# Optimization experiments

Hardware: AMD Instinct MI355X
Metric: run time of the kernel (lower is better)

The kernel has to match this reference:

```python
import jax, jax.numpy as jnp
import numpy as np

B, S, D, H, L = 2, 4096, 768, 12, 2
DH = D // H
W = 256            # one-sided sliding window (longformer-base attention_window=512)
VOCAB = 50265
SEP_ID = 2
N_SEPS = 63
G = N_SEPS + 1     # global tokens: <s> at pos 0 + all </s> separators
FF = 4 * D
C = 7
NEG = -1e9


def layer_norm(x, s, b, eps=1e-5):
    m = x.mean(-1, keepdims=True)
    v = ((x - m) ** 2).mean(-1, keepdims=True)
    return (x - m) * jax.lax.rsqrt(v + eps) * s + b


def setup_inputs():
    key = jax.random.key(0)
    keys = iter(jax.random.split(key, 64))
    def nrm(shape, sd=0.02):
        return jax.random.normal(next(keys), shape, jnp.float32) * sd
    input_ids = jax.random.randint(next(keys), (B, S), 5, VOCAB, dtype=jnp.int32)
    input_ids = input_ids.at[:, 0].set(0)  # <s>
    sep_pos = (jnp.arange(N_SEPS) + 1) * (S // (N_SEPS + 1))  # 64,128,...,4032
    input_ids = input_ids.at[:, sep_pos].set(SEP_ID)
    return dict(
        emb_tok=nrm((VOCAB, D)), emb_pos=nrm((S, D)),
        ln_e_s=jnp.ones((D,)), ln_e_b=jnp.zeros((D,)),
        Wq=nrm((L, D, D)), bq=jnp.zeros((L, D)),
        Wk=nrm((L, D, D)), bk=jnp.zeros((L, D)),
        Wv=nrm((L, D, D)), bv=jnp.zeros((L, D)),
        Wqg=nrm((L, D, D)), bqg=jnp.zeros((L, D)),
        Wkg=nrm((L, D, D)), bkg=jnp.zeros((L, D)),
        Wvg=nrm((L, D, D)), bvg=jnp.zeros((L, D)),
        Wo=nrm((L, D, D)), bo=jnp.zeros((L, D)),
        ln1_s=jnp.ones((L, D)), ln1_b=jnp.zeros((L, D)),
        Wf1=nrm((L, D, FF)), bf1=jnp.zeros((L, FF)),
        Wf2=nrm((L, FF, D)), bf2=jnp.zeros((L, D)),
        ln2_s=jnp.ones((L, D)), ln2_b=jnp.zeros((L, D)),
        Wc=nrm((D, C)), bc=jnp.zeros((C,)),
        input_ids=input_ids,
        attention_mask=jnp.ones((B, S), jnp.int32),
        left_overlap=2, right_overlap=2,
    )


def _forward(emb_tok, emb_pos, ln_e_s, ln_e_b, Wq, bq, Wk, bk, Wv, bv,
             Wqg, bqg, Wkg, bkg, Wvg, bvg, Wo, bo, ln1_s, ln1_b,
             Wf1, bf1, Wf2, bf2, ln2_s, ln2_b, Wc, bc,
             input_ids, attention_mask, left_overlap, right_overlap):
    pos = jnp.arange(S)
    # global attention mask: first token + every </s> token (as in the torch forward)
    g_mask = (input_ids == SEP_ID) | (pos[None, :] == 0)                         # [B,S]
    idx_g = jax.vmap(lambda m: jnp.nonzero(m, size=G, fill_value=0)[0])(g_mask)  # [B,G]
    am = attention_mask.astype(jnp.float32)
    key_local_ok = am * (1.0 - g_mask.astype(jnp.float32))  # globals excluded from windowed keys
    nb = S // W
    band_idx = jnp.arange(nb)[:, None] * W + jnp.arange(3 * W)[None, :]  # [nb,3W] into W-padded seq
    rel = jnp.arange(3 * W)[None, :] - W - jnp.arange(W)[:, None]        # key_pos - query_pos
    band_ok = (jnp.abs(rel) <= W)[None, None, None]                       # [1,1,1,W,3W]
    kv_ok = jnp.pad(key_local_ok, ((0, 0), (W, W)))[:, band_idx] > 0      # [B,nb,3W]
    mask = band_ok & kv_ok[:, None, :, None, :]                           # [B,1,nb,W,3W]
    scale = float(DH) ** -0.5
    bix = jnp.arange(B)[:, None]

    x = emb_tok[input_ids] + emb_pos[None]
    x = layer_norm(x, ln_e_s, ln_e_b)
    for l in range(L):
        q = (x @ Wq[l] + bq[l]).reshape(B, S, H, DH)
        k = (x @ Wk[l] + bk[l]).reshape(B, S, H, DH)
        v = (x @ Wv[l] + bv[l]).reshape(B, S, H, DH)
        kb = jnp.pad(k, ((0, 0), (W, W), (0, 0), (0, 0)))[:, band_idx]    # [B,nb,3W,H,DH]
        vb = jnp.pad(v, ((0, 0), (W, W), (0, 0), (0, 0)))[:, band_idx]
        s_band = jnp.einsum('bnqhd,bnkhd->bhnqk', q.reshape(B, nb, W, H, DH), kb) * scale
        s_band = jnp.where(mask, s_band, NEG)
        kg = jnp.take_along_axis(k, idx_g[:, :, None, None], axis=1)      # [B,G,H,DH]
        vg = jnp.take_along_axis(v, idx_g[:, :, None, None], axis=1)
        s_glob = jnp.einsum('bqhd,bghd->bhqg', q, kg) * scale
        probs = jax.nn.softmax(
            jnp.concatenate([s_band.reshape(B, H, S, 3 * W), s_glob], axis=-1), axis=-1)
        out = (jnp.einsum('bhnqk,bnkhd->bnqhd',
                          probs[..., :3 * W].reshape(B, H, nb, W, 3 * W), vb).reshape(B, S, H, DH)
               + jnp.einsum('bhqg,bghd->bqhd', probs[..., 3 * W:], vg)).reshape(B, S, D)
        # global query rows: full attention over all tokens with dedicated global projections
        xg = jnp.take_along_axis(x, idx_g[:, :, None], axis=1)            # [B,G,D]
        qg = (xg @ Wqg[l] + bqg[l]).reshape(B, G, H, DH)
        kga = (x @ Wkg[l] + bkg[l]).reshape(B, S, H, DH)
        vga = (x @ Wvg[l] + bvg[l]).reshape(B, S, H, DH)
        sg = jnp.where(am[:, None, None, :] > 0,
                       jnp.einsum('bghd,bshd->bhgs', qg, kga) * scale, NEG)
        og = jnp.einsum('bhgs,bshd->bghd', jax.nn.softmax(sg, axis=-1), vga).reshape(B, G, D)
        out = out.at[bix, idx_g].set(og)
        x = layer_norm(x + out @ Wo[l] + bo[l], ln1_s[l], ln1_b[l])
        x = layer_norm(x + jax.nn.gelu(x @ Wf1[l] + bf1[l]) @ Wf2[l] + bf2[l], ln2_s[l], ln2_b[l])
    # classification head (eval-mode dropout = identity). Faithful to the torch code,
    # which gathers hidden states at token POSITION j for j in [left, n_seps - right).
    core = x[:, left_overlap:N_SEPS - right_overlap, :]                    # [B, n_core, D]
    return (core @ Wc + bc).reshape(-1, C)


def reference(emb_tok, emb_pos, ln_e_s, ln_e_b, Wq, bq, Wk, bk, Wv, bv,
              Wqg, bqg, Wkg, bkg, Wvg, bvg, Wo, bo, ln1_s, ln1_b,
              Wf1, bf1, Wf2, bf2, ln2_s, ln2_b, Wc, bc,
              input_ids, attention_mask, left_overlap, right_overlap):
    return _forward(emb_tok, emb_pos, ln_e_s, ln_e_b, Wq, bq, Wk, bk, Wv, bv,
                    Wqg, bqg, Wkg, bkg, Wvg, bvg, Wo, bo, ln1_s, ln1_b,
                    Wf1, bf1, Wf2, bf2, ln2_s, ln2_b, Wc, bc,
                    input_ids, attention_mask, left_overlap, right_overlap)
```

## Files before the change

kernel.cpp:

```cpp
#include <hip/hip_runtime.h>
#include <hip/hip_bf16.h>
#include <stdint.h>

#define B_ 2
#define S_ 4096
#define D_ 768
#define H_ 12
#define DH_ 64
#define L_ 2
#define W_ 256
#define G_ 64
#define FF_ 3072
#define C_ 7
#define SEP_ 2
#define NEG_ (-1000000000.0f)
#define NC_ 16

typedef __attribute__((ext_vector_type(8))) short short8;
typedef __attribute__((ext_vector_type(4))) float f32x4;

__device__ __forceinline__ float bfu2f(unsigned short u) {
    return __uint_as_float(((unsigned int)u) << 16);
}
__device__ __forceinline__ unsigned short f2bfu(float f) {
    unsigned int x = __float_as_uint(f);
    unsigned int r = (x + 0x7fffu + ((x >> 16) & 1u)) >> 16;
    return (unsigned short)r;
}
__device__ __forceinline__ float gelu_tanh(float v) {
    float c = 0.7978845608028654f * (v + 0.044715f * v * v * v);
    return 0.5f * v * (1.0f + tanhf(c));
}

__device__ __forceinline__ void gl16(const unsigned short* g, unsigned short* l) {
    __builtin_amdgcn_global_load_lds(
        (const __attribute__((address_space(1))) unsigned int*)g,
        (__attribute__((address_space(3))) unsigned int*)l,
        16, 0, 0);
}

__device__ __forceinline__ void xcd_remap(int& bx, int& by, int& bz) {
    int nx = gridDim.x, ny = gridDim.y, nz = gridDim.z;
    int flat = bx + nx * (by + ny * bz);
    int nxz = nx * nz;
    int xcd = flat & 7;
    int n = flat >> 3;
    int band = n / nxz;
    int r = n - band * nxz;
    by = xcd * (ny >> 3) + band;
    bz = r / nx;
    bx = r - bz * nx;
}

#define GEMM_COMPUTE()                                                                   \
    {                                                                                    \
        short8 af[4], bf[4];                                                             \
        _Pragma("unroll")                                                                \
        for (int i_ = 0; i_ < 4; i_++)                                                   \
            af[i_] = *(const short8*)&As[(wm + i_ * 16 + l16) * 32 + quad * 8];          \
        _Pragma("unroll")                                                                \
        for (int j_ = 0; j_ < 4; j_++)                                                   \
            bf[j_] = *(const short8*)&Bs[(wn + j_ * 16 + l16) * 32 + quad * 8];          \
        _Pragma("unroll")                                                                \
        for (int i_ = 0; i_ < 4; i_++)                                                   \
            _Pragma("unroll")                                                            \
            for (int j_ = 0; j_ < 4; j_++)                                               \
                acc[i_][j_] = __builtin_amdgcn_mfma_f32_16x16x32_bf16(af[i_], bf[j_],    \
                                                                      acc[i_][j_], 0, 0, 0); \
    }

__global__ __launch_bounds__(256) void k_wtrans(
    const float* __restrict__ src, unsigned short* __restrict__ dst,
    int K, int N, size_t dstStride) {
    int l = blockIdx.z;
    src += (size_t)l * K * N;
    dst += (size_t)l * dstStride;
    __shared__ unsigned short tile[32][36];
    int t = threadIdx.x;
    int r = t >> 3, c4 = (t & 7) << 2;
    int k0 = blockIdx.y << 5, n0 = blockIdx.x << 5;
    float4 v = *(const float4*)(src + (size_t)(k0 + r) * N + n0 + c4);
    tile[c4 + 0][r] = f2bfu(v.x);
    tile[c4 + 1][r] = f2bfu(v.y);
    tile[c4 + 2][r] = f2bfu(v.z);
    tile[c4 + 3][r] = f2bfu(v.w);
    __syncthreads();
    ushort4 o;
    o.x = tile[r][c4 + 0]; o.y = tile[r][c4 + 1];
    o.z = tile[r][c4 + 2]; o.w = tile[r][c4 + 3];
    *(ushort4*)(dst + (size_t)(n0 + r) * K + k0 + c4) = o;
}

__global__ __launch_bounds__(256) void k_embed_ln(
    const int* __restrict__ ids, const float* __restrict__ etok,
    const float* __restrict__ epos, const float* __restrict__ lns,
    const float* __restrict__ lnb, float* __restrict__ x,
    unsigned short* __restrict__ xb) {
    int row = (blockIdx.x << 2) + (threadIdx.x >> 6);
    int lane = threadIdx.x & 63;
    int s = row & (S_ - 1);
    int id = ids[row];
    const float4* ep = (const float4*)(etok + (size_t)id * D_);
    const float4* pp = (const float4*)(epos + (size_t)s * D_);
    float4 a[3];
    float sum = 0.f, sum2 = 0.f;
#pragma unroll
    for (int i = 0; i < 3; i++) {
        float4 ev = ep[lane + i * 64];
        float4 pv = pp[lane + i * 64];
        ev.x += pv.x; ev.y += pv.y; ev.z += pv.z; ev.w += pv.w;
        a[i] = ev;
        sum  += ev.x + ev.y + ev.z + ev.w;
        sum2 += ev.x * ev.x + ev.y * ev.y + ev.z * ev.z + ev.w * ev.w;
    }
#pragma unroll
    for (int off = 1; off < 64; off <<= 1) {
        sum += __shfl_xor(sum, off);
        sum2 += __shfl_xor(sum2, off);
    }
    float mean = sum * (1.0f / D_);
    float var = sum2 * (1.0f / D_) - mean * mean;
    float rs = rsqrtf(var + 1e-5f);
    float4* xp = (float4*)(x + (size_t)row * D_);
#pragma unroll
    for (int i = 0; i < 3; i++) {
        float4 g = *(const float4*)(lns + lane * 4 + i * 256);
        float4 bb = *(const float4*)(lnb + lane * 4 + i * 256);
        float4 v;
        v.x = (a[i].x - mean) * rs * g.x + bb.x;
        v.y = (a[i].y - mean) * rs * g.y + bb.y;
        v.z = (a[i].z - mean) * rs * g.z + bb.z;
        v.w = (a[i].w - mean) * rs * g.w + bb.w;
        xp[lane + i * 64] = v;
        ushort4 u; u.x = f2bfu(v.x); u.y = f2bfu(v.y); u.z = f2bfu(v.z); u.w = f2bfu(v.w);
        *(ushort4*)(xb + (size_t)row * D_ + lane * 4 + i * 256) = u;
    }
}

__global__ __launch_bounds__(256) void k_add_ln(
    float* __restrict__ x, const float* __restrict__ y, const float* __restrict__ y2,
    const float* __restrict__ lns, const float* __restrict__ lnb,
    unsigned short* __restrict__ xb) {
    int row = (blockIdx.x << 2) + (threadIdx.x >> 6);
    int lane = threadIdx.x & 63;
    float4* xp = (float4*)(x + (size_t)row * D_);
    const float4* yp = (const float4*)(y + (size_t)row * D_);
    const float4* y2p = y2 ? (const float4*)(y2 + (size_t)row * D_) : nullptr;
    float4 a[3];
    float sum = 0.f, sum2 = 0.f;
#pragma unroll
    for (int i = 0; i < 3; i++) {
        float4 xv = xp[lane + i * 64];
        float4 yv = yp[lane + i * 64];
        xv.x += yv.x; xv.y += yv.y; xv.z += yv.z; xv.w += yv.w;
        if (y2p) {
            float4 zv = y2p[lane + i * 64];
            xv.x += zv.x; xv.y += zv.y; xv.z += zv.z; xv.w += zv.w;
        }
        a[i] = xv;
        sum  += xv.x + xv.y + xv.z + xv.w;
        sum2 += xv.x * xv.x + xv.y * xv.y + xv.z * xv.z + xv.w * xv.w;
    }
#pragma unroll
    for (int off = 1; off < 64; off <<= 1) {
        sum += __shfl_xor(sum, off);
        sum2 += __shfl_xor(sum2, off);
    }
    float mean = sum * (1.0f / D_);
    float var = sum2 * (1.0f / D_) - mean * mean;
    float rs = rsqrtf(var + 1e-5f);
#pragma unroll
    for (int i = 0; i < 3; i++) {
        float4 g = *(const float4*)(lns + lane * 4 + i * 256);
        float4 bb = *(const float4*)(lnb + lane * 4 + i * 256);
        float4 v;
        v.x = (a[i].x - mean) * rs * g.x + bb.x;
        v.y = (a[i].y - mean) * rs * g.y + bb.y;
        v.z = (a[i].z - mean) * rs * g.z + bb.z;
        v.w = (a[i].w - mean) * rs * g.w + bb.w;
        xp[lane + i * 64] = v;
        ushort4 u; u.x = f2bfu(v.x); u.y = f2bfu(v.y); u.z = f2bfu(v.z); u.w = f2bfu(v.w);
        *(ushort4*)(xb + (size_t)row * D_ + lane * 4 + i * 256) = u;
    }
}

__global__ __launch_bounds__(256) void k_idx(const int* __restrict__ ids, int* __restrict__ idxg) {
    int b = blockIdx.x;
    int t = threadIdx.x;
    __shared__ int cnt[256];
    __shared__ int totsh;
    int loc[16];
    int n = 0;
#pragma unroll
    for (int i = 0; i < 16; i++) {
        int s = t * 16 + i;
        if (s == 0 || ids[b * S_ + s] == SEP_) loc[n++] = s;
    }
    cnt[t] = n;
    __syncthreads();
    int base = 0;
    for (int u = 0; u < t; u++) base += cnt[u];
    for (int i = 0; i < n; i++) {
        int o = base + i;
        if (o < G_) idxg[b * G_ + o] = loc[i];
    }
    if (t == 255) totsh = base + n;
    __syncthreads();
    if (t == 0)
        for (int o = totsh; o < G_; o++) idxg[b * G_ + o] = 0;
}

__global__ __launch_bounds__(256) void k_gemm_mfma(
    const unsigned short* __restrict__ A, const unsigned short* __restrict__ Wt,
    const float* __restrict__ Wf, const float* __restrict__ bias,
    float* __restrict__ Cf, float* __restrict__ Cf2, unsigned short* __restrict__ Cb,
    int M, int N, int K, int act) {
    __shared__ __align__(16) unsigned short As[128 * 32];
    __shared__ __align__(16) unsigned short Bs[128 * 32];
    int bx = blockIdx.x, by = blockIdx.y, bz = blockIdx.z;
    xcd_remap(bx, by, bz);
    int t = threadIdx.x;
    int wave = t >> 6, lane = t & 63, l16 = lane & 15, quad = lane >> 4;
    int m0 = by << 7, n0 = bx << 7;
    int wm = (wave >> 1) << 6, wn = (wave & 1) << 6;
    int slice = bz;
    int kper = K / gridDim.z;
    int kbeg = slice * kper, kend = kbeg + kper;
    f32x4 acc[4][4];
#pragma unroll
    for (int i = 0; i < 4; i++)
#pragma unroll
        for (int j = 0; j < 4; j++) acc[i][j] = (f32x4){0.f, 0.f, 0.f, 0.f};

    int ch = wave * 128 + lane;
    int srow = ch >> 2, spos = ch & 3;
    unsigned short* al0 = As + wave * 1024;
    unsigned short* al1 = As + wave * 1024 + 512;
    unsigned short* bl0 = Bs + wave * 1024;
    unsigned short* bl1 = Bs + wave * 1024 + 512;
    const unsigned short* ag = A + (size_t)(m0 + srow) * K + kbeg + spos * 8;

    if (Wt) {
        const unsigned short* bg = Wt + (size_t)(n0 + srow) * K + kbeg + spos * 8;
        for (int k0 = kbeg; k0 < kend; k0 += 32) {
            gl16(ag, al0);
            gl16(ag + (size_t)16 * K, al1);
            gl16(bg, bl0);
            gl16(bg + (size_t)16 * K, bl1);
            __syncthreads();
            GEMM_COMPUTE();
            __syncthreads();
            ag += 32; bg += 32;
        }
    } else {
        int bn = t & 127, bkh = (t >> 7) << 4;
        for (int k0 = kbeg; k0 < kend; k0 += 32) {
            gl16(ag, al0);
            gl16(ag + (size_t)16 * K, al1);
            const float* bp = Wf + (size_t)(k0 + bkh) * N + n0 + bn;
            unsigned int pk[8];
#pragma unroll
            for (int i = 0; i < 8; i++) {
                unsigned int lo = f2bfu(bp[(size_t)(2 * i) * N]);
                unsigned int hi = f2bfu(bp[(size_t)(2 * i + 1) * N]);
                pk[i] = lo | (hi << 16);
            }
            *(uint4*)&Bs[bn * 32 + bkh] = *(uint4*)&pk[0];
            *(uint4*)&Bs[bn * 32 + bkh + 8] = *(uint4*)&pk[4];
            __syncthreads();
            GEMM_COMPUTE();
            __syncthreads();
            ag += 32;
        }
    }
    float bj[4];
#pragma unroll
    for (int j = 0; j < 4; j++) bj[j] = (slice == 0) ? bias[n0 + wn + j * 16 + l16] : 0.f;
    float* outp = (slice == 0) ? Cf : Cf2;
#pragma unroll
    for (int i = 0; i < 4; i++)
#pragma unroll
        for (int j = 0; j < 4; j++) {
            int col = n0 + wn + j * 16 + l16;
#pragma unroll
            for (int r = 0; r < 4; r++) {
                int row = m0 + wm + i * 16 + quad * 4 + r;
                float v = acc[i][j][r] + bj[j];
                if (act) v = gelu_tanh(v);
                if (outp) outp[(size_t)row * N + col] = v;
                else      Cb[(size_t)row * N + col] = f2bfu(v);
            }
        }
}

struct P5 {
    const unsigned short* Wt[5];
    const float* Wf[5];
    const float* bias[5];
    unsigned short* out[5];
};
__global__ __launch_bounds__(256) void k_gemm_qkv5(
    const unsigned short* __restrict__ A, P5 p) {
    __shared__ __align__(16) unsigned short As[128 * 32];
    __shared__ __align__(16) unsigned short Bs[128 * 32];
    int bx = blockIdx.x, by = blockIdx.y, bz = blockIdx.z;
    xcd_remap(bx, by, bz);
    const unsigned short* __restrict__ Wt = p.Wt[bz];
    const float* __restrict__ Wf = p.Wf[bz];
    const float* __restrict__ bias = p.bias[bz];
    unsigned short* __restrict__ Cb = p.out[bz];
    const int N = D_, K = D_;
    int t = threadIdx.x;
    int wave = t >> 6, lane = t & 63, l16 = lane & 15, quad = lane >> 4;
    int m0 = by << 7, n0 = bx << 7;
    int wm = (wave >> 1) << 6, wn = (wave & 1) << 6;
    f32x4 acc[4][4];
#pragma unroll
    for (int i = 0; i < 4; i++)
#pragma unroll
        for (int j = 0; j < 4; j++) acc[i][j] = (f32x4){0.f, 0.f, 0.f, 0.f};

    int ch = wave * 128 + lane;
    int srow = ch >> 2, spos = ch & 3;
    unsigned short* al0 = As + wave * 1024;
    unsigned short* al1 = As + wave * 1024 + 512;
    unsigned short* bl0 = Bs + wave * 1024;
    unsigned short* bl1 = Bs + wave * 1024 + 512;
    const unsigned short* ag = A + (size_t)(m0 + srow) * K + spos * 8;

    if (Wt) {
        const unsigned short* bg = Wt + (size_t)(n0 + srow) * K + spos * 8;
        for (int k0 = 0; k0 < K; k0 += 32) {
            gl16(ag + k0, al0);
            gl16(ag + 16 * K + k0, al1);
            gl16(bg + k0, bl0);
            gl16(bg + 16 * K + k0, bl1);
            __syncthreads();
            GEMM_COMPUTE();
            __syncthreads();
        }
    } else {
        int bn = t & 127, bkh = (t >> 7) << 4;
        for (int k0 = 0; k0 < K; k0 += 32) {
            gl16(ag + k0, al0);
            gl16(ag + 16 * K + k0, al1);
            const float* bp = Wf + (size_t)(k0 + bkh) * N + n0 + bn;
            unsigned int pk[8];
#pragma unroll
            for (int i = 0; i < 8; i++) {
                unsigned int lo = f2bfu(bp[(size_t)(2 * i) * N]);
                unsigned int hi = f2bfu(bp[(size_t)(2 * i + 1) * N]);
                pk[i] = lo | (hi << 16);
            }
            *(uint4*)&Bs[bn * 32 + bkh] = *(uint4*)&pk[0];
            *(uint4*)&Bs[bn * 32 + bkh + 8] = *(uint4*)&pk[4];
            __syncthreads();
            GEMM_COMPUTE();
            __syncthreads();
        }
    }
    float bj[4];
#pragma unroll
    for (int j = 0; j < 4; j++) bj[j] = bias[n0 + wn + j * 16 + l16];
#pragma unroll
    for (int i = 0; i < 4; i++)
#pragma unroll
        for (int j = 0; j < 4; j++) {
            int col = n0 + wn + j * 16 + l16;
#pragma unroll
            for (int r = 0; r < 4; r++) {
                int row = m0 + wm + i * 16 + quad * 4 + r;
                float v = acc[i][j][r] + bj[j];
                size_t adr = ((((size_t)(row >> 12)) * H_ + (col >> 6)) * S_ +
                              (row & (S_ - 1))) * DH_ + (col & 63);
                Cb[adr] = f2bfu(v);
            }
        }
}

__global__ __launch_bounds__(256) void k_lattn(
    const unsigned short* __restrict__ q, const unsigned short* __restrict__ k,
    const unsigned short* __restrict__ v, const int* __restrict__ ids,
    const int* __restrict__ am, const int* __restrict__ idxg,
    unsigned short* __restrict__ Tb) {
    int s0 = blockIdx.x << 6, h = blockIdx.y, b = blockIdx.z;
    int t = threadIdx.x;
    int wave = t >> 6, lane = t & 63, l16 = lane & 15, quad = lane >> 4;

    __shared__ unsigned short Ks[64][72];
    __shared__ unsigned short Vt[64][72];
    __shared__ unsigned short Ps[64][72];
    __shared__ unsigned char keyok[64];

    const size_t headbase = (((size_t)b * H_) + h) * S_;
    int qrow = s0 + wave * 16 + l16;
    const unsigned short* qptr = q + (headbase + qrow) * DH_;
    short8 qa0 = *(const short8*)(qptr + quad * 8);
    short8 qa1 = *(const short8*)(qptr + 32 + quad * 8);

    f32x4 O[4];
#pragma unroll
    for (int nf = 0; nf < 4; nf++) O[nf] = (f32x4){0.f, 0.f, 0.f, 0.f};
    float m_run[4] = {-3.4e38f, -3.4e38f, -3.4e38f, -3.4e38f};
    float l_run[4] = {0.f, 0.f, 0.f, 0.f};

    int kbase = s0 - 256;
    int sr = t >> 2, sc = t & 3;

    for (int tile = 0; tile < 10; tile++) {
        int sK, sclamp; bool okf;
        if (tile < 9) {
            sK = kbase + tile * 64 + sr;
            bool inr = (sK >= 0) && (sK < S_);
            sclamp = inr ? sK : 0;
            okf = inr && (am[b * S_ + sclamp] != 0) &&
                  !((ids[b * S_ + sclamp] == SEP_) || (sK == 0));
        } else {
            sK = idxg[b * G_ + sr];
            sclamp = sK; okf = true;
        }
        if (sc == 0) keyok[sr] = okf ? 1 : 0;
        const unsigned short* srcK = k + (headbase + sclamp) * DH_;
        const unsigned short* srcV = v + (headbase + sclamp) * DH_;
        uint4 k0v = *(const uint4*)(srcK + sc * 8);
        uint4 k1v = *(const uint4*)(srcK + (sc + 4) * 8);
        uint4 v0v = *(const uint4*)(srcV + sc * 8);
        uint4 v1v = *(const uint4*)(srcV + (sc + 4) * 8);
        *(uint4*)&Ks[sr][sc * 8] = k0v;
        *(uint4*)&Ks[sr][(sc + 4) * 8] = k1v;
        const unsigned int* vw0 = (const unsigned int*)&v0v;
        const unsigned int* vw1 = (const unsigned int*)&v1v;
#pragma unroll
        for (int i = 0; i < 4; i++) {
            Vt[sc * 8 + 2 * i][sr]      = (unsigned short)(vw0[i] & 0xffff);
            Vt[sc * 8 + 2 * i + 1][sr]  = (unsigned short)(vw0[i] >> 16);
            Vt[(sc + 4) * 8 + 2 * i][sr]     = (unsigned short)(vw1[i] & 0xffff);
            Vt[(sc + 4) * 8 + 2 * i + 1][sr] = (unsigned short)(vw1[i] >> 16);
        }
        __syncthreads();

        f32x4 Sf[4];
#pragma unroll
        for (int nf = 0; nf < 4; nf++) {
            short8 b0 = *(const short8*)&Ks[nf * 16 + l16][quad * 8];
            short8 b1 = *(const short8*)&Ks[nf * 16 + l16][32 + quad * 8];
            f32x4 a = (f32x4){0.f, 0.f, 0.f, 0.f};
            a = __builtin_amdgcn_mfma_f32_16x16x32_bf16(qa0, b0, a, 0, 0, 0);
            a = __builtin_amdgcn_mfma_f32_16x16x32_bf16(qa1, b1, a, 0, 0, 0);
            Sf[nf] = a;
        }
        int ktb = kbase + tile * 64;
        bool kval[4];
#pragma unroll
        for (int nf = 0; nf < 4; nf++) kval[nf] = (tile == 9) || (keyok[nf * 16 + l16] != 0);
        float P_[4][4];
        float mt[4];
#pragma unroll
        for (int r = 0; r < 4; r++) {
            int qs = s0 + wave * 16 + quad * 4 + r;
            float mx = -3.4e38f;
#pragma unroll
            for (int nf = 0; nf < 4; nf++) {
                int ks2 = ktb + nf * 16 + l16;
                bool ok = kval[nf] && ((tile == 9) || (ks2 >= qs - 256 && ks2 <= qs + 256));
                float sv = ok ? Sf[nf][r] * 0.125f : NEG_;
                P_[nf][r] = sv;
                mx = fmaxf(mx, sv);
            }
            mt[r] = mx;
        }
#pragma unroll
        for (int off = 1; off < 16; off <<= 1)
#pragma unroll
            for (int r = 0; r < 4; r++) mt[r] = fmaxf(mt[r], __shfl_xor(mt[r], off));
        float alpha[4], lt[4];
#pragma unroll
        for (int r = 0; r < 4; r++) {
            float mn = fmaxf(m_run[r], mt[r]);
            alpha[r] = __expf(m_run[r] - mn);
            m_run[r] = mn; lt[r] = 0.f;
        }
#pragma unroll
        for (int nf = 0; nf < 4; nf++)
#pragma unroll
            for (int r = 0; r < 4; r++) {
                float p = (P_[nf][r] > -1.0e8f) ? __expf(P_[nf][r] - m_run[r]) : 0.f;
                P_[nf][r] = p; lt[r] += p;
            }
#pragma unroll
        for (int off = 1; off < 16; off <<= 1)
#pragma unroll
            for (int r = 0; r < 4; r++) lt[r] += __shfl_xor(lt[r], off);
#pragma unroll
        for (int r = 0; r < 4; r++) l_run[r] = l_run[r] * alpha[r] + lt[r];
#pragma unroll
        for (int nf = 0; nf < 4; nf++) {
            O[nf][0] *= alpha[0]; O[nf][1] *= alpha[1];
            O[nf][2] *= alpha[2]; O[nf][3] *= alpha[3];
        }
#pragma unroll
        for (int nf = 0; nf < 4; nf++)
#pragma unroll
            for (int r = 0; r < 4; r++)
                Ps[wave * 16 + quad * 4 + r][nf * 16 + l16] = f2bfu(P_[nf][r]);
#pragma unroll
        for (int hh = 0; hh < 2; hh++) {
            short8 pa = *(const short8*)&Ps[wave * 16 + l16][hh * 32 + quad * 8];
#pragma unroll
            for (int nf = 0; nf < 4; nf++) {
                short8 vb8 = *(const short8*)&Vt[nf * 16 + l16][hh * 32 + quad * 8];
                O[nf] = __builtin_amdgcn_mfma_f32_16x16x32_bf16(pa, vb8, O[nf], 0, 0, 0);
            }
        }
        __syncthreads();
    }
#pragma unroll
    for (int r = 0; r < 4; r++) {
        int qs = s0 + wave * 16 + quad * 4 + r;
        float invl = 1.0f / l_run[r];
        size_t base = ((size_t)(b * S_ + qs)) * D_ + h * DH_;
#pragma unroll
        for (int nf = 0; nf < 4; nf++)
            Tb[base + nf * 16 + l16] = f2bfu(O[nf][r] * invl);
    }
}

__global__ __launch_bounds__(256) void k_gattn_part(
    const unsigned short* __restrict__ qg, const unsigned short* __restrict__ kga,
    const unsigned short* __restrict__ vga, const int* __restrict__ am,
    float* __restrict__ Opart, float* __restrict__ mbuf, float* __restrict__ lbuf) {
    int c = blockIdx.x, h = blockIdx.y, b = blockIdx.z;
    int t = threadIdx.x;
    int wave = t >> 6, lane = t & 63, l16 = lane & 15, quad = lane >> 4;

    __shared__ unsigned short Ks[64][72];
    __shared__ unsigned short Vt[64][72];
    __shared__ unsigned short Ps[64][72];
    __shared__ unsigned char keyok[64];

    const size_t headbase = (((size_t)b * H_) + h) * S_;
    int grow = wave * 16 + l16;
    const unsigned short* qptr = qg + ((size_t)(b * G_ + grow)) * D_ + h * DH_;
    short8 qa0 = *(const short8*)(qptr + quad * 8);
    short8 qa1 = *(const short8*)(qptr + 32 + quad * 8);

    f32x4 O[4];
#pragma unroll
    for (int nf = 0; nf < 4; nf++) O[nf] = (f32x4){0.f, 0.f, 0.f, 0.f};
    float m_run[4] = {-3.4e38f, -3.4e38f, -3.4e38f, -3.4e38f};
    float l_run[4] = {0.f, 0.f, 0.f, 0.f};

    int kbase = c * 256;
    int sr = t >> 2, sc = t & 3;

    for (int tile = 0; tile < 4; tile++) {
        int sK = kbase + tile * 64 + sr;
        if (sc == 0) keyok[sr] = (am[b * S_ + sK] != 0) ? 1 : 0;
        const unsigned short* srcK = kga + (headbase + sK) * DH_;
        const unsigned short* srcV = vga + (headbase + sK) * DH_;
        uint4 k0v = *(const uint4*)(srcK + sc * 8);
        uint4 k1v = *(const uint4*)(srcK + (sc + 4) * 8);
        uint4 v0v = *(const uint4*)(srcV + sc * 8);
        uint4 v1v = *(const uint4*)(srcV + (sc + 4) * 8);
        *(uint4*)&Ks[sr][sc * 8] = k0v;
        *(uint4*)&Ks[sr][(sc + 4) * 8] = k1v;
        const unsigned int* vw0 = (const unsigned int*)&v0v;
        const unsigned int* vw1 = (const unsigned int*)&v1v;
#pragma unroll
        for (int i = 0; i < 4; i++) {
            Vt[sc * 8 + 2 * i][sr]      = (unsigned short)(vw0[i] & 0xffff);
            Vt[sc * 8 + 2 * i + 1][sr]  = (unsigned short)(vw0[i] >> 16);
            Vt[(sc + 4) * 8 + 2 * i][sr]     = (unsigned short)(vw1[i] & 0xffff);
            Vt[(sc + 4) * 8 + 2 * i + 1][sr] = (unsigned short)(vw1[i] >> 16);
        }
        __syncthreads();

        f32x4 Sf[4];
#pragma unroll
        for (int nf = 0; nf < 4; nf++) {
            short8 b0 = *(const short8*)&Ks[nf * 16 + l16][quad * 8];
            short8 b1 = *(const short8*)&Ks[nf * 16 + l16][32 + quad * 8];
            f32x4 a = (f32x4){0.f, 0.f, 0.f, 0.f};
            a = __builtin_amdgcn_mfma_f32_16x16x32_bf16(qa0, b0, a, 0, 0, 0);
            a = __builtin_amdgcn_mfma_f32_16x16x32_bf16(qa1, b1, a, 0, 0, 0);
            Sf[nf] = a;
        }
        bool kval[4];
#pragma unroll
        for (int nf = 0; nf < 4; nf++) kval[nf] = (keyok[nf * 16 + l16] != 0);
        float P_[4][4];
        float mt[4];
#pragma unroll
        for (int r = 0; r < 4; r++) {
            float mx = -3.4e38f;
#pragma unroll
            for (int nf = 0; nf < 4; nf++) {
                float sv = kval[nf] ? Sf[nf][r] * 0.125f : NEG_;
                P_[nf][r] = sv;
                mx = fmaxf(mx, sv);
            }
            mt[r] = mx;
        }
#pragma unroll
        for (int off = 1; off < 16; off <<= 1)
#pragma unroll
            for (int r = 0; r < 4; r++) mt[r] = fmaxf(mt[r], __shfl_xor(mt[r], off));
        float alpha[4], lt[4];
#pragma unroll
        for (int r = 0; r < 4; r++) {
            float mn = fmaxf(m_run[r], mt[r]);
            alpha[r] = __expf(m_run[r] - mn);
            m_run[r] = mn; lt[r] = 0.f;
        }
#pragma unroll
        for (int nf = 0; nf < 4; nf++)
#pragma unroll
            for (int r = 0; r < 4; r++) {
                float p = (P_[nf][r] > -1.0e8f) ? __expf(P_[nf][r] - m_run[r]) : 0.f;
                P_[nf][r] = p; lt[r] += p;
            }
#pragma unroll
        for (int off = 1; off < 16; off <<= 1)
#pragma unroll
            for (int r = 0; r < 4; r++) lt[r] += __shfl_xor(lt[r], off);
#pragma unroll
        for (int r = 0; r < 4; r++) l_run[r] = l_run[r] * alpha[r] + lt[r];
#pragma unroll
        for (int nf = 0; nf < 4; nf++) {
            O[nf][0] *= alpha[0]; O[nf][1] *= alpha[1];
            O[nf][2] *= alpha[2]; O[nf][3] *= alpha[3];
        }
#pragma unroll
        for (int nf = 0; nf < 4; nf++)
#pragma unroll
            for (int r = 0; r < 4; r++)
                Ps[wave * 16 + quad * 4 + r][nf * 16 + l16] = f2bfu(P_[nf][r]);
#pragma unroll
        for (int hh = 0; hh < 2; hh++) {
            short8 pa = *(const short8*)&Ps[wave * 16 + l16][hh * 32 + quad * 8];
#pragma unroll
            for (int nf = 0; nf < 4; nf++) {
                short8 vb8 = *(const short8*)&Vt[nf * 16 + l16][hh * 32 + quad * 8];
                O[nf] = __builtin_amdgcn_mfma_f32_16x16x32_bf16(pa, vb8, O[nf], 0, 0, 0);
            }
        }
        __syncthreads();
    }
    size_t bhc = ((size_t)(b * H_ + h)) * NC_ + c;
#pragma unroll
    for (int r = 0; r < 4; r++) {
        int row = wave * 16 + quad * 4 + r;
#pragma unroll
        for (int nf = 0; nf < 4; nf++)
            Opart[bhc * (G_ * DH_) + (size_t)row * DH_ + nf * 16 + l16] = O[nf][r];
        if (l16 == 0) {
            mbuf[bhc * G_ + row] = m_run[r];
            lbuf[bhc * G_ + row] = l_run[r];
        }
    }
}

__global__ __launch_bounds__(64) void k_gattn_comb(
    const float* __restrict__ Opart, const float* __restrict__ mbuf,
    const float* __restrict__ lbuf, const int* __restrict__ idxg,
    unsigned short* __restrict__ Tb) {
    int g = blockIdx.x, h = blockIdx.y, b = blockIdx.z;
    int d = threadIdx.x;
    size_t bh = (size_t)(b * H_ + h);
    float M = -3.4e38f;
    float mv[NC_];
#pragma unroll
    for (int c = 0; c < NC_; c++) {
        mv[c] = mbuf[(bh * NC_ + c) * G_ + g];
        M = fmaxf(M, mv[c]);
    }
    float L = 0.f, o = 0.f;
#pragma unroll
    for (int c = 0; c < NC_; c++) {
        float e = __expf(mv[c] - M);
        L += lbuf[(bh * NC_ + c) * G_ + g] * e;
        o += Opart[(bh * NC_ + c) * (G_ * DH_) + (size_t)g * DH_ + d] * e;
    }
    int srow = idxg[b * G_ + g];
    Tb[((size_t)(b * S_ + srow)) * D_ + h * DH_ + d] = f2bfu(o / L);
}

__global__ __launch_bounds__(256) void k_gemm(
    const float* __restrict__ A, const float* __restrict__ Bw,
    const float* __restrict__ bias, float* __restrict__ Cf,
    unsigned short* __restrict__ Cb, int M, int N, int K, int act) {
    __shared__ float As[16][68];
    __shared__ float Bs[16][68];
    int tl = threadIdx.x;
    int tx = tl & 15, ty = tl >> 4;
    int m0 = blockIdx.y << 6, n0 = blockIdx.x << 6;
    float c[4][4] = {{0.f}};
    int arow = tl >> 2, akk = (tl & 3) << 2;
    int bkk = tl >> 4, bcol = (tl & 15) << 2;
    for (int k0 = 0; k0 < K; k0 += 16) {
        float4 a4 = *(const float4*)(A + (size_t)(m0 + arow) * K + k0 + akk);
        As[akk + 0][arow] = a4.x; As[akk + 1][arow] = a4.y;
        As[akk + 2][arow] = a4.z; As[akk + 3][arow] = a4.w;
        float4 b4 = *(const float4*)(Bw + (size_t)(k0 + bkk) * N + n0 + bcol);
        Bs[bkk][bcol + 0] = b4.x; Bs[bkk][bcol + 1] = b4.y;
        Bs[bkk][bcol + 2] = b4.z; Bs[bkk][bcol + 3] = b4.w;
        __syncthreads();
#pragma unroll
        for (int kk = 0; kk < 16; kk++) {
            float4 av = *(const float4*)&As[kk][ty << 2];
            float4 bv = *(const float4*)&Bs[kk][tx << 2];
            float aa[4] = {av.x, av.y, av.z, av.w};
            float bb[4] = {bv.x, bv.y, bv.z, bv.w};
#pragma unroll
            for (int i = 0; i < 4; i++)
#pragma unroll
                for (int j = 0; j < 4; j++) c[i][j] += aa[i] * bb[j];
        }
        __syncthreads();
    }
    float bias4[4];
#pragma unroll
    for (int j = 0; j < 4; j++) bias4[j] = bias[n0 + (tx << 2) + j];
#pragma unroll
    for (int i = 0; i < 4; i++) {
        int mrow = m0 + (ty << 2) + i;
        float v0 = c[i][0] + bias4[0], v1 = c[i][1] + bias4[1];
        float v2 = c[i][2] + bias4[2], v3 = c[i][3] + bias4[3];
        if (act) { v0 = gelu_tanh(v0); v1 = gelu_tanh(v1); v2 = gelu_tanh(v2); v3 = gelu_tanh(v3); }
        if (Cf) {
            float4 o; o.x = v0; o.y = v1; o.z = v2; o.w = v3;
            *(float4*)(Cf + (size_t)mrow * N + n0 + (tx << 2)) = o;
        } else {
            ushort4 o; o.x = f2bfu(v0); o.y = f2bfu(v1); o.z = f2bfu(v2); o.w = f2bfu(v3);
            *(ushort4*)(Cb + (size_t)mrow * N + n0 + (tx << 2)) = o;
        }
    }
}

__global__ __launch_bounds__(256) void k_gather_xg(
    const float* __restrict__ x, const int* __restrict__ idxg, float* __restrict__ xg) {
    int bg = blockIdx.x;
    int b = bg / G_;
    int srow = idxg[bg];
    for (int d = threadIdx.x; d < D_; d += 256)
        xg[(size_t)bg * D_ + d] = x[((size_t)(b * S_ + srow)) * D_ + d];
}

__global__ __launch_bounds__(256) void k_classifier(
    const float* __restrict__ x, const float* __restrict__ Wc,
    const float* __restrict__ bc, const int* __restrict__ lo_p,
    int rows_pb, float* __restrict__ out) {
    int r = blockIdx.x;
    int b = r / rows_pb, i = r % rows_pb;
    int s = lo_p[0] + i;
    int t = threadIdx.x;
    __shared__ float xr[D_];
    __shared__ float red[256];
    const float* xrow = x + ((size_t)(b * S_ + s)) * D_;
    for (int d = t; d < D_; d += 256) xr[d] = xrow[d];
    __syncthreads();
    for (int c = 0; c < C_; c++) {
        float loc = 0.f;
        for (int d = t; d < D_; d += 256) loc += xr[d] * Wc[d * C_ + c];
        red[t] = loc; __syncthreads();
        for (int o = 128; o; o >>= 1) { if (t < o) red[t] += red[t + o]; __syncthreads(); }
        if (t == 0) out[r * C_ + c] = red[0] + bc[c];
        __syncthreads();
    }
}

extern "C" void kernel_launch(void* const* d_in, const int* in_sizes, int n_in,
                              void* d_out, int out_size, void* d_ws, size_t ws_size,
                              hipStream_t stream) {
    (void)in_sizes; (void)n_in;
    const float* emb_tok = (const float*)d_in[0];
    const float* emb_pos = (const float*)d_in[1];
    const float* ln_e_s = (const float*)d_in[2];
    const float* ln_e_b = (const float*)d_in[3];
    const float* Wq  = (const float*)d_in[4];
    const float* bq  = (const float*)d_in[5];
    const float* Wk  = (const float*)d_in[6];
    const float* bk  = (const float*)d_in[7];
    const float* Wv  = (const float*)d_in[8];
    const float* bv  = (const float*)d_in[9];
    const float* Wqg = (const float*)d_in[10];
    const float* bqg = (const float*)d_in[11];
    const float* Wkg = (const float*)d_in[12];
    const float* bkg = (const float*)d_in[13];
    const float* Wvg = (const float*)d_in[14];
    const float* bvg = (const float*)d_in[15];
    const float* Wo  = (const float*)d_in[16];
    const float* bo  = (const float*)d_in[17];
    const float* ln1_s = (const float*)d_in[18];
    const float* ln1_b = (const float*)d_in[19];
    const float* Wf1 = (const float*)d_in[20];
    const float* bf1 = (const float*)d_in[21];
    const float* Wf2 = (const float*)d_in[22];
    const float* bf2 = (const float*)d_in[23];
    const float* ln2_s = (const float*)d_in[24];
    const float* ln2_b = (const float*)d_in[25];
    const float* Wc  = (const float*)d_in[26];
    const float* bc  = (const float*)d_in[27];
    const int* input_ids = (const int*)d_in[28];
    const int* attn_mask = (const int*)d_in[29];
    const int* lo        = (const int*)d_in[30];

    const size_t SZB = (size_t)B_ * S_ * D_;
    const size_t D2 = (size_t)D_ * D_;
    const size_t PL = 6 * D2 + 2 * (size_t)D_ * FF_;
    uint8_t* w = (uint8_t*)d_ws;
    float*          x    = (float*)w;
    unsigned short* xb   = (unsigned short*)(w + 4 * SZB);
    float*          P    = (float*)(w + 6 * SZB);
    unsigned short* qb   = (unsigned short*)(w + 10 * SZB);
    unsigned short* kb   = (unsigned short*)(w + 12 * SZB);
    unsigned short* vb   = (unsigned short*)(w + 14 * SZB);
    unsigned short* kgab = (unsigned short*)(w + 16 * SZB);
    unsigned short* vgab = (unsigned short*)(w + 18 * SZB);
    unsigned short* Hb   = (unsigned short*)(w + 10 * SZB);
    unsigned short* Tb   = (unsigned short*)(w + 20 * SZB);
    float* xg = (float*)(w + 22 * SZB);
    unsigned short* qgb = (unsigned short*)(w + 22 * SZB + (size_t)B_ * G_ * D_ * 4);
    int* idxg = (int*)(w + 22 * SZB + (size_t)B_ * G_ * D_ * 4 + (size_t)B_ * G_ * D_ * 2);
    float* Opart = (float*)(w + 23 * SZB);
    float* mbuf  = (float*)(w + 24 * SZB);
    float* lbuf  = mbuf + (size_t)B_ * H_ * NC_ * G_;

    const size_t P2_OFF = 24 * SZB + (1u << 20);
    const size_t WB_OFF = P2_OFF + 4 * SZB;
    const size_t NEED_P2 = WB_OFF;
    const size_t NEED_W = WB_OFF + L_ * PL * 2;
    float* P2 = (float*)(w + P2_OFF);
    unsigned short* wb = (unsigned short*)(w + WB_OFF);
    const int useW = (ws_size >= NEED_W) ? 1 : 0;
    const int useSplit = (ws_size >= NEED_P2) ? 1 : 0;

    const int BS = B_ * S_;

    if (useW) {
        k_wtrans<<<dim3(D_/32, D_/32, L_), 256, 0, stream>>>(Wq,  wb + 0*D2, D_, D_, PL);
        k_wtrans<<<dim3(D_/32, D_/32, L_), 256, 0, stream>>>(Wk,  wb + 1*D2, D_, D_, PL);
        k_wtrans<<<dim3(D_/32, D_/32, L_), 256, 0, stream>>>(Wv,  wb + 2*D2, D_, D_, PL);
        k_wtrans<<<dim3(D_/32, D_/32, L_), 256, 0, stream>>>(Wkg, wb + 3*D2, D_, D_, PL);
        k_wtrans<<<dim3(D_/32, D_/32, L_), 256, 0, stream>>>(Wvg, wb + 4*D2, D_, D_, PL);
        k_wtrans<<<dim3(D_/32, D_/32, L_), 256, 0, stream>>>(Wo,  wb + 5*D2, D_, D_, PL);
        k_wtrans<<<dim3(FF_/32, D_/32, L_), 256, 0, stream>>>(Wf1, wb + 6*D2, D_, FF_, PL);
        k_wtrans<<<dim3(D_/32, FF_/32, L_), 256, 0, stream>>>(Wf2, wb + 6*D2 + (size_t)D_*FF_, FF_, D_, PL);
    }

    k_embed_ln<<<BS / 4, 256, 0, stream>>>(input_ids, emb_tok, emb_pos, ln_e_s, ln_e_b, x, xb);
    k_idx<<<B_, 256, 0, stream>>>(input_ids, idxg);

    dim3 g_d(D_ / 128, BS / 128);
    dim3 g_ds(D_ / 128, BS / 128, useSplit ? 2 : 1);
    dim3 g_d5(D_ / 128, BS / 128, 5);
    dim3 g_ff(FF_ / 128, BS / 128);
    dim3 g_qg(D_ / 64, (B_ * G_) / 64);

    for (int l = 0; l < L_; l++) {
        const unsigned short* wbl = wb + (size_t)l * PL;
        P5 p5;
        p5.Wf[0] = Wq  + (size_t)l * D2;  p5.bias[0] = bq  + l * D_;  p5.out[0] = qb;
        p5.Wf[1] = Wk  + (size_t)l * D2;  p5.bias[1] = bk  + l * D_;  p5.out[1] = kb;
        p5.Wf[2] = Wv  + (size_t)l * D2;  p5.bias[2] = bv  + l * D_;  p5.out[2] = vb;
        p5.Wf[3] = Wkg + (size_t)l * D2;  p5.bias[3] = bkg + l * D_;  p5.out[3] = kgab;
        p5.Wf[4] = Wvg + (size_t)l * D2;  p5.bias[4] = bvg + l * D_;  p5.out[4] = vgab;
        for (int i = 0; i < 5; i++) p5.Wt[i] = useW ? (wbl + (size_t)i * D2) : nullptr;
        const float* Wqg_l = Wqg + (size_t)l * D2;
        const float* Wo_l  = Wo  + (size_t)l * D2;
        const float* Wf1_l = Wf1 + (size_t)l * D_ * FF_;
        const float* Wf2_l = Wf2 + (size_t)l * FF_ * D_;
        const unsigned short* Wo_t  = useW ? (wbl + 5 * D2) : nullptr;
        const unsigned short* Wf1_t = useW ? (wbl + 6 * D2) : nullptr;
        const unsigned short* Wf2_t = useW ? (wbl + 6 * D2 + (size_t)D_ * FF_) : nullptr;

        k_gemm_qkv5<<<g_d5, 256, 0, stream>>>(xb, p5);
        k_lattn<<<dim3(S_ / 64, H_, B_), 256, 0, stream>>>(qb, kb, vb, input_ids, attn_mask, idxg, Tb);
        k_gather_xg<<<B_ * G_, 256, 0, stream>>>(x, idxg, xg);
        k_gemm<<<g_qg, 256, 0, stream>>>(xg, Wqg_l, bqg + l * D_, nullptr, qgb, B_ * G_, D_, D_, 0);
        k_gattn_part<<<dim3(NC_, H_, B_), 256, 0, stream>>>(qgb, kgab, vgab, attn_mask, Opart, mbuf, lbuf);
        k_gattn_comb<<<dim3(G_, H_, B_), 64, 0, stream>>>(Opart, mbuf, lbuf, idxg, Tb);
        k_gemm_mfma<<<g_ds, 256, 0, stream>>>(Tb, Wo_t, Wo_l, bo + l * D_, P, P2, nullptr, BS, D_, D_, 0);
        k_add_ln<<<BS / 4, 256, 0, stream>>>(x, P, useSplit ? P2 : nullptr, ln1_s + l * D_, ln1_b + l * D_, xb);
        k_gemm_mfma<<<g_ff, 256, 0, stream>>>(xb, Wf1_t, Wf1_l, bf1 + l * FF_, nullptr, nullptr, Hb, BS, FF_, D_, 1);
        k_gemm_mfma<<<g_ds, 256, 0, stream>>>(Hb, Wf2_t, Wf2_l, bf2 + l * D_, P, P2, nullptr, BS, D_, FF_, 0);
        k_add_ln<<<BS / 4, 256, 0, stream>>>(x, P, useSplit ? P2 : nullptr, ln2_s + l * D_, ln2_b + l * D_, xb);
    }

    int rows = out_size / C_;
    int rows_pb = rows / B_;
    k_classifier<<<rows, 256, 0, stream>>>(x, Wc, bc, lo, rows_pb, (float*)d_out);
}
```

Before: 1.160 ms.

## Double-buffer LDS tiles in MFMA GEMMs and use exp-based GELU

The bf16 pre-transposed weight paths of the generic and QKV GEMM kernels now keep two LDS buffers. The next K-slice is issued via global_load_lds while MFMAs run on the current one, and there is one vmcnt wait plus barrier per iteration instead of two syncthreads. This aims to hide global-load latency behind compute, at the cost of doubling LDS use per block, which may lower occupancy. GELU-tanh is also rewritten as the equivalent sigmoid form v/(1+exp(-2c)) using the fast __expf intrinsic to cheapen the FFN epilogue, with slightly different rounding.

```diff
diff --git a/kernel.cpp b/kernel.cpp
--- a/kernel.cpp
+++ b/kernel.cpp
@@ -28,8 +28,8 @@
     return (unsigned short)r;
 }
 __device__ __forceinline__ float gelu_tanh(float v) {
-    float c = 0.7978845608028654f * (v + 0.044715f * v * v * v);
-    return 0.5f * v * (1.0f + tanhf(c));
+    float u = 1.5957691216057308f * v + 0.0713548162726f * v * v * v;
+    return v / (1.0f + __expf(-u));
 }
 
 __device__ __forceinline__ void gl16(const unsigned short* g, unsigned short* l) {
@@ -52,21 +52,27 @@
     bx = r - bz * nx;
 }
 
-#define GEMM_COMPUTE()                                                                   \
+#define GEMM_COMPUTE(Ab, Bb)                                                             \
     {                                                                                    \
         short8 af[4], bf[4];                                                             \
         _Pragma("unroll")                                                                \
         for (int i_ = 0; i_ < 4; i_++)                                                   \
-            af[i_] = *(const short8*)&As[(wm + i_ * 16 + l16) * 32 + quad * 8];          \
+            af[i_] = *(const short8*)&(Ab)[(wm + i_ * 16 + l16) * 32 + quad * 8];        \
         _Pragma("unroll")                                                                \
         for (int j_ = 0; j_ < 4; j_++)                                                   \
-            bf[j_] = *(const short8*)&Bs[(wn + j_ * 16 + l16) * 32 + quad * 8];          \
+            bf[j_] = *(const short8*)&(Bb)[(wn + j_ * 16 + l16) * 32 + quad * 8];        \
         _Pragma("unroll")                                                                \
         for (int i_ = 0; i_ < 4; i_++)                                                   \
             _Pragma("unroll")                                                            \
             for (int j_ = 0; j_ < 4; j_++)                                               \
                 acc[i_][j_] = __builtin_amdgcn_mfma_f32_16x16x32_bf16(af[i_], bf[j_],    \
                                                                       acc[i_][j_], 0, 0, 0); \
+    }
+
+#define WAIT_VM0_BARRIER()                                   \
+    {                                                        \
+        asm volatile("s_waitcnt vmcnt(0)" ::: "memory");     \
+        __builtin_amdgcn_s_barrier();                        \
     }
 
 __global__ __launch_bounds__(256) void k_wtrans(
@@ -215,8 +221,8 @@
     const float* __restrict__ Wf, const float* __restrict__ bias,
     float* __restrict__ Cf, float* __restrict__ Cf2, unsigned short* __restrict__ Cb,
     int M, int N, int K, int act) {
-    __shared__ __align__(16) unsigned short As[128 * 32];
-    __shared__ __align__(16) unsigned short Bs[128 * 32];
+    __shared__ __align__(16) unsigned short As[2 * 128 * 32];
+    __shared__ __align__(16) unsigned short Bs[2 * 128 * 32];
     int bx = blockIdx.x, by = blockIdx.y, bz = blockIdx.z;
     xcd_remap(bx, by, bz);
     int t = threadIdx.x;
@@ -234,29 +240,36 @@
 
     int ch = wave * 128 + lane;
     int srow = ch >> 2, spos = ch & 3;
-    unsigned short* al0 = As + wave * 1024;
-    unsigned short* al1 = As + wave * 1024 + 512;
-    unsigned short* bl0 = Bs + wave * 1024;
-    unsigned short* bl1 = Bs + wave * 1024 + 512;
     const unsigned short* ag = A + (size_t)(m0 + srow) * K + kbeg + spos * 8;
 
     if (Wt) {
         const unsigned short* bg = Wt + (size_t)(n0 + srow) * K + kbeg + spos * 8;
+        gl16(ag, As + wave * 1024);
+        gl16(ag + (size_t)16 * K, As + wave * 1024 + 512);
+        gl16(bg, Bs + wave * 1024);
+        gl16(bg + (size_t)16 * K, Bs + wave * 1024 + 512);
+        WAIT_VM0_BARRIER();
+        int cur = 0;
         for (int k0 = kbeg; k0 < kend; k0 += 32) {
-            gl16(ag, al0);
-            gl16(ag + (size_t)16 * K, al1);
-            gl16(bg, bl0);
-            gl16(bg + (size_t)16 * K, bl1);
-            __syncthreads();
-            GEMM_COMPUTE();
-            __syncthreads();
-            ag += 32; bg += 32;
+            int koff = k0 + 32 - kbeg;
+            if (k0 + 32 < kend) {
+                int nb = cur ^ 1;
+                gl16(ag + koff, As + nb * 4096 + wave * 1024);
+                gl16(ag + koff + (size_t)16 * K, As + nb * 4096 + wave * 1024 + 512);
+                gl16(bg + koff, Bs + nb * 4096 + wave * 1024);
+                gl16(bg + koff + (size_t)16 * K, Bs + nb * 4096 + wave * 1024 + 512);
+            }
+            const unsigned short* Ab = As + cur * 4096;
+            const unsigned short* Bb = Bs + cur * 4096;
+            GEMM_COMPUTE(Ab, Bb);
+            WAIT_VM0_BARRIER();
+            cur ^= 1;
         }
     } else {
         int bn = t & 127, bkh = (t >> 7) << 4;
         for (int k0 = kbeg; k0 < kend; k0 += 32) {
-            gl16(ag, al0);
-            gl16(ag + (size_t)16 * K, al1);
+            gl16(ag + (k0 - kbeg), As + wave * 1024);
+            gl16(ag + (k0 - kbeg) + (size_t)16 * K, As + wave * 1024 + 512);
             const float* bp = Wf + (size_t)(k0 + bkh) * N + n0 + bn;
             unsigned int pk[8];
 #pragma unroll
@@ -268,9 +281,8 @@
             *(uint4*)&Bs[bn * 32 + bkh] = *(uint4*)&pk[0];
             *(uint4*)&Bs[bn * 32 + bkh + 8] = *(uint4*)&pk[4];
             __syncthreads();
-            GEMM_COMPUTE();
+            GEMM_COMPUTE(As, Bs);
             __syncthreads();
-            ag += 32;
         }
     }
     float bj[4];
@@ -301,8 +313,8 @@
 };
 __global__ __launch_bounds__(256) void k_gemm_qkv5(
     const unsigned short* __restrict__ A, P5 p) {
-    __shared__ __align__(16) unsigned short As[128 * 32];
-    __shared__ __align__(16) unsigned short Bs[128 * 32];
+    __shared__ __align__(16) unsigned short As[2 * 128 * 32];
+    __shared__ __align__(16) unsigned short Bs[2 * 128 * 32];
     int bx = blockIdx.x, by = blockIdx.y, bz = blockIdx.z;
     xcd_remap(bx, by, bz);
     const unsigned short* __restrict__ Wt = p.Wt[bz];
@@ -322,28 +334,36 @@
 
     int ch = wave * 128 + lane;
     int srow = ch >> 2, spos = ch & 3;
-    unsigned short* al0 = As + wave * 1024;
-    unsigned short* al1 = As + wave * 1024 + 512;
-    unsigned short* bl0 = Bs + wave * 1024;
-    unsigned short* bl1 = Bs + wave * 1024 + 512;
     const unsigned short* ag = A + (size_t)(m0 + srow) * K + spos * 8;
 
     if (Wt) {
         const unsigned short* bg = Wt + (size_t)(n0 + srow) * K + spos * 8;
+        gl16(ag, As + wave * 1024);
+        gl16(ag + (size_t)16 * K, As + wave * 1024 + 512);
+        gl16(bg, Bs + wave * 1024);
+        gl16(bg + (size_t)16 * K, Bs + wave * 1024 + 512);
+        WAIT_VM0_BARRIER();
+        int cur = 0;
         for (int k0 = 0; k0 < K; k0 += 32) {
-            gl16(ag + k0, al0);
-            gl16(ag + 16 * K + k0, al1);
-            gl16(bg + k0, bl0);
-            gl16(bg + 16 * K + k0, bl1);
-            __syncthreads();
-            GEMM_COMPUTE();
-            __syncthreads();
+            int koff = k0 + 32;
+            if (koff < K) {
+                int nb = cur ^ 1;
+                gl16(ag + koff, As + nb * 4096 + wave * 1024);
+                gl16(ag + koff + (size_t)16 * K, As + nb * 4096 + wave * 1024 + 512);
+                gl16(bg + koff, Bs + nb * 4096 + wave * 1024);
+                gl16(bg + koff + (size_t)16 * K, Bs + nb * 4096 + wave * 1024 + 512);
+            }
+            const unsigned short* Ab = As + cur * 4096;
+            const unsigned short* Bb = Bs + cur * 4096;
+            GEMM_COMPUTE(Ab, Bb);
+            WAIT_VM0_BARRIER();
+            cur ^= 1;
         }
     } else {
         int bn = t & 127, bkh = (t >> 7) << 4;
         for (int k0 = 0; k0 < K; k0 += 32) {
-            gl16(ag + k0, al0);
-            gl16(ag + 16 * K + k0, al1);
+            gl16(ag + k0, As + wave * 1024);
+            gl16(ag + k0 + (size_t)16 * K, As + wave * 1024 + 512);
             const float* bp = Wf + (size_t)(k0 + bkh) * N + n0 + bn;
             unsigned int pk[8];
 #pragma unroll
@@ -355,7 +375,7 @@
             *(uint4*)&Bs[bn * 32 + bkh] = *(uint4*)&pk[0];
             *(uint4*)&Bs[bn * 32 + bkh + 8] = *(uint4*)&pk[4];
             __syncthreads();
-            GEMM_COMPUTE();
+            GEMM_COMPUTE(As, Bs);
             __syncthreads();
         }
     }
```

Result: faster. 1.126 ms (-2.9%).
